# Optimization experiments

Hardware: AMD Instinct MI355X
Metric: run time of the kernel (lower is better)

Reference implementation:

```python
import jax, jax.numpy as jnp
import numpy as np

IN_FEATURES = 28 * 28  # 784
OUT_FEATURES = 1000    # label_num
GRID_SIZE = 10
SPLINE_ORDER = 3
GRID_RANGE = (0.0, 1.0)


def _make_grid(dtype):
    # grid = arange(-spline_order, grid_size+spline_order+1) * h + grid_range[0]
    h = (GRID_RANGE[1] - GRID_RANGE[0]) / GRID_SIZE
    return (jnp.arange(-SPLINE_ORDER, GRID_SIZE + SPLINE_ORDER + 1, dtype=dtype) * h
            + GRID_RANGE[0])  # [grid_size + 2*spline_order + 1] = [17]


def b_splines(x):
    # x: [B, in]; returns [B, in, grid_size + spline_order] = [B, 784, 13]
    grid = _make_grid(x.dtype)
    g = grid[None, None, :]          # broadcast over batch and in_features
    xu = x[:, :, None]               # [B, in, 1]
    bases = ((xu >= g[..., :-1]) & (xu < g[..., 1:])).astype(x.dtype)
    for k in range(1, SPLINE_ORDER + 1):
        left = (xu - g[..., :-(k + 1)]) / (g[..., k:-1] - g[..., :-(k + 1)])
        right = (g[..., k + 1:] - xu) / (g[..., k + 1:] - g[..., 1:-k])
        bases = left * bases[..., :-1] + right * bases[..., 1:]
    return bases


def setup_inputs() -> dict:
    key = jax.random.key(0)
    k1, k2, k3, k4 = jax.random.split(key, 4)
    B = 8192
    x = jax.random.uniform(k1, (B, 1, 28, 28), dtype=jnp.float32)  # values in grid range [0,1]
    base_weight = 0.03 * jax.random.normal(k2, (OUT_FEATURES, IN_FEATURES), dtype=jnp.float32)
    spline_weight = 0.02 * jax.random.normal(
        k3, (OUT_FEATURES, IN_FEATURES, GRID_SIZE + SPLINE_ORDER), dtype=jnp.float32)
    spline_scaler = 1.0 + 0.05 * jax.random.normal(k4, (OUT_FEATURES, IN_FEATURES), dtype=jnp.float32)
    return {"x": x, "base_weight": base_weight,
            "spline_weight": spline_weight, "spline_scaler": spline_scaler}


def reference(x, base_weight, spline_weight, spline_scaler):
    B = x.shape[0]
    xf = x.reshape(B, IN_FEATURES)                       # Flatten
    # base branch: SiLU(x) @ base_weight.T
    base_out = jnp.einsum('bi,oi->bo', jax.nn.silu(xf), base_weight)
    # spline branch: B-spline basis contracted with scaled spline weights
    bases = b_splines(xf)                                # [B, in, 13]
    sw = spline_weight * spline_scaler[..., None]        # [out, in, 13]
    spline_out = jnp.einsum('big,oig->bo', bases, sw)
    logits = base_out + spline_out                       # [B, out]
    return jax.nn.log_softmax(logits, axis=1)
```

## Files before the change

### kernel.cpp

```cpp
#include <hip/hip_runtime.h>
#include <hip/hip_bf16.h>
#include <stdint.h>

#define IN_F 784
#define OUT_F 1000
#define CH 16
#define KDIM (IN_F * CH)
#define MDIM 8192
#define NPAD 1024
#define KSTEPS (KDIM / 64)

typedef __attribute__((ext_vector_type(8))) short bf16x8;
typedef __attribute__((ext_vector_type(4))) float f32x4;

__device__ __forceinline__ unsigned short f2bf(float f) {
    unsigned u = __float_as_uint(f);
    u = (u + 0x7FFFu + ((u >> 16) & 1u)) >> 16;
    return (unsigned short)u;
}
__device__ __forceinline__ unsigned pack2(float lo, float hi) {
    return (unsigned)f2bf(lo) | ((unsigned)f2bf(hi) << 16);
}

__global__ void prep_A(const float* __restrict__ X, unsigned short* __restrict__ A) {
    int tid = blockIdx.x * 256 + threadIdx.x;
    int b = tid / IN_F;
    int i = tid - b * IN_F;
    float x = X[tid];
    float s = x / (1.0f + __expf(-x));
    float tf = x * 10.0f;
    float cf = floorf(tf);
    cf = fminf(fmaxf(cf, 0.0f), 9.0f);
    int c = (int)cf;
    float u = tf - cf;
    float u2 = u * u, u3 = u2 * u;
    float om = 1.0f - u;
    const float s6 = 1.0f / 6.0f;
    float b0 = om * om * om * s6;
    float b1 = (3.0f * u3 - 6.0f * u2 + 4.0f) * s6;
    float b2 = (-3.0f * u3 + 3.0f * u2 + 3.0f * u + 1.0f) * s6;
    float b3 = u3 * s6;
    float v[16];
    v[0] = s;
    #pragma unroll
    for (int k = 0; k < 13; ++k) {
        float val = (k == c)     ? b0 : 0.0f;
        val       = (k == c + 1) ? b1 : val;
        val       = (k == c + 2) ? b2 : val;
        val       = (k == c + 3) ? b3 : val;
        v[1 + k] = val;
    }
    v[14] = 0.0f; v[15] = 0.0f;
    unsigned w[8];
    #pragma unroll
    for (int j = 0; j < 8; ++j) w[j] = pack2(v[2 * j], v[2 * j + 1]);
    uint4* dst = (uint4*)(A + (size_t)b * KDIM + (size_t)i * CH);
    dst[0] = make_uint4(w[0], w[1], w[2], w[3]);
    dst[1] = make_uint4(w[4], w[5], w[6], w[7]);
}

__global__ void prep_W(const float* __restrict__ BW, const float* __restrict__ SW,
                       const float* __restrict__ SC, unsigned short* __restrict__ Wm) {
    int tid = blockIdx.x * 256 + threadIdx.x;
    int o = tid / IN_F;
    int i = tid - o * IN_F;
    unsigned w[8];
    if (o < OUT_F) {
        float bw = BW[o * IN_F + i];
        float sc = SC[o * IN_F + i];
        const float* swp = SW + (size_t)(o * IN_F + i) * 13;
        float v[16];
        v[0] = bw;
        #pragma unroll
        for (int g = 0; g < 13; ++g) v[1 + g] = swp[g] * sc;
        v[14] = 0.0f; v[15] = 0.0f;
        #pragma unroll
        for (int j = 0; j < 8; ++j) w[j] = pack2(v[2 * j], v[2 * j + 1]);
    } else {
        #pragma unroll
        for (int j = 0; j < 8; ++j) w[j] = 0u;
    }
    uint4* dst = (uint4*)(Wm + (size_t)o * KDIM + (size_t)i * CH);
    dst[0] = make_uint4(w[0], w[1], w[2], w[3]);
    dst[1] = make_uint4(w[4], w[5], w[6], w[7]);
}

__global__ void __launch_bounds__(256) kan_gemm(const unsigned short* __restrict__ A,
                                                const unsigned short* __restrict__ W,
                                                float* __restrict__ out) {
    __shared__ __align__(16) unsigned char smem[32768];
    const int t = threadIdx.x;
    const int bid = blockIdx.x;
    const int mb = bid >> 3, nb = bid & 7;
    const int bRow = mb * 128, bCol = nb * 128;
    const int w = t >> 6;
    const int lane = t & 63;
    const int lrow = lane & 15;
    const int lk = lane >> 4;
    const int sx = lrow & 7;
    const int r8 = t >> 3;
    const int p = t & 7;
    const int wm = w >> 1, wn = w & 1;

    const char* Ab = (const char*)A;
    const char* Wb = (const char*)W;

    f32x4 acc[4][4];
    #pragma unroll
    for (int m = 0; m < 4; ++m)
        #pragma unroll
        for (int n = 0; n < 4; ++n)
            acc[m][n] = (f32x4){0.f, 0.f, 0.f, 0.f};

    for (int ks = 0; ks < KSTEPS; ++ks) {
        const int k0 = ks * 64;
        #pragma unroll
        for (int it = 0; it < 4; ++it) {
            int r = it * 32 + r8;
            int sc = p ^ (r & 7);
            const char* src = Ab + ((size_t)(bRow + r) * KDIM + k0) * 2 + sc * 16;
            __builtin_amdgcn_global_load_lds(
                (const __attribute__((address_space(1))) char*)src,
                (__attribute__((address_space(3))) char*)&smem[it * 4096 + w * 1024],
                16, 0, 0);
        }
        #pragma unroll
        for (int it = 0; it < 4; ++it) {
            int r = it * 32 + r8;
            int sc = p ^ (r & 7);
            const char* src = Wb + ((size_t)(bCol + r) * KDIM + k0) * 2 + sc * 16;
            __builtin_amdgcn_global_load_lds(
                (const __attribute__((address_space(1))) char*)src,
                (__attribute__((address_space(3))) char*)&smem[16384 + it * 4096 + w * 1024],
                16, 0, 0);
        }
        __syncthreads();

        #pragma unroll
        for (int kk = 0; kk < 2; ++kk) {
            bf16x8 af[4], bfr[4];
            #pragma unroll
            for (int m = 0; m < 4; ++m) {
                int row = wm * 64 + m * 16 + lrow;
                int ch = (kk * 4 + lk) ^ sx;
                af[m] = *(const bf16x8*)&smem[row * 128 + ch * 16];
            }
            #pragma unroll
            for (int n = 0; n < 4; ++n) {
                int row = wn * 64 + n * 16 + lrow;
                int ch = (kk * 4 + lk) ^ sx;
                bfr[n] = *(const bf16x8*)&smem[16384 + row * 128 + ch * 16];
            }
            #pragma unroll
            for (int m = 0; m < 4; ++m)
                #pragma unroll
                for (int n = 0; n < 4; ++n)
                    acc[m][n] = __builtin_amdgcn_mfma_f32_16x16x32_bf16(af[m], bfr[n], acc[m][n], 0, 0, 0);
        }
        __syncthreads();
    }

    #pragma unroll
    for (int m = 0; m < 4; ++m) {
        int grow0 = bRow + wm * 64 + m * 16 + lk * 4;
        #pragma unroll
        for (int n = 0; n < 4; ++n) {
            int gcol = bCol + wn * 64 + n * 16 + lrow;
            if (gcol < OUT_F) {
                #pragma unroll
                for (int j = 0; j < 4; ++j)
                    out[(size_t)(grow0 + j) * OUT_F + gcol] = acc[m][n][j];
            }
        }
    }
}

__global__ void logsoftmax_inplace(float* __restrict__ out) {
    const int b = blockIdx.x;
    float* row = out + (size_t)b * OUT_F;
    const int t = threadIdx.x;
    const int ln = t & 63, wv = t >> 6;
    float v[4];
    #pragma unroll
    for (int j = 0; j < 4; ++j) {
        int idx = t + 256 * j;
        v[j] = (idx < OUT_F) ? row[idx] : -1e30f;
    }
    float m = fmaxf(fmaxf(v[0], v[1]), fmaxf(v[2], v[3]));
    #pragma unroll
    for (int off = 32; off > 0; off >>= 1) m = fmaxf(m, __shfl_xor(m, off, 64));
    __shared__ float red[4];
    if (ln == 0) red[wv] = m;
    __syncthreads();
    m = fmaxf(fmaxf(red[0], red[1]), fmaxf(red[2], red[3]));
    float s = 0.f;
    #pragma unroll
    for (int j = 0; j < 4; ++j) {
        int idx = t + 256 * j;
        if (idx < OUT_F) s += __expf(v[j] - m);
    }
    #pragma unroll
    for (int off = 32; off > 0; off >>= 1) s += __shfl_xor(s, off, 64);
    __syncthreads();
    if (ln == 0) red[wv] = s;
    __syncthreads();
    s = red[0] + red[1] + red[2] + red[3];
    float lse = m + logf(s);
    #pragma unroll
    for (int j = 0; j < 4; ++j) {
        int idx = t + 256 * j;
        if (idx < OUT_F) row[idx] = v[j] - lse;
    }
}

extern "C" void kernel_launch(void* const* d_in, const int* in_sizes, int n_in,
                              void* d_out, int out_size, void* d_ws, size_t ws_size,
                              hipStream_t stream) {
    const float* x  = (const float*)d_in[0];
    const float* bw = (const float*)d_in[1];
    const float* sw = (const float*)d_in[2];
    const float* sc = (const float*)d_in[3];
    float* out = (float*)d_out;

    unsigned short* A  = (unsigned short*)d_ws;
    unsigned short* Wm = (unsigned short*)((char*)d_ws + (size_t)MDIM * KDIM * 2);

    prep_A<<<dim3(MDIM * IN_F / 256), 256, 0, stream>>>(x, A);
    prep_W<<<dim3(NPAD * IN_F / 256), 256, 0, stream>>>(bw, sw, sc, Wm);
    kan_gemm<<<dim3((MDIM / 128) * (NPAD / 128)), 256, 0, stream>>>(A, Wm, out);
    logsoftmax_inplace<<<dim3(MDIM), 256, 0, stream>>>(out);
}
```

Measured before the change: 462.2 us.

## Split GEMM K-loop across two warp groups per block with LDS reduction

The GEMM block grows to 512 threads, with two 256-thread groups each handling half of the K range in its own 32KB LDS region. The partial accumulators are summed through LDS before the store. The block-to-tile mapping is also remapped so consecutive blocks share the same N column tile, which should improve L2 reuse of W. The goal is more warps per CU to hide load latency, at the cost of double LDS use, which may lower the number of resident blocks, plus a reduction epilogue.

```diff
diff --git a/kernel.cpp b/kernel.cpp
--- a/kernel.cpp
+++ b/kernel.cpp
@@ -9,6 +9,7 @@
 #define MDIM 8192
 #define NPAD 1024
 #define KSTEPS (KDIM / 64)
+#define KHALF (KSTEPS / 2)
 
 typedef __attribute__((ext_vector_type(8))) short bf16x8;
 typedef __attribute__((ext_vector_type(4))) float f32x4;
@@ -85,22 +86,27 @@
     dst[1] = make_uint4(w[4], w[5], w[6], w[7]);
 }
 
-__global__ void __launch_bounds__(256) kan_gemm(const unsigned short* __restrict__ A,
-                                                const unsigned short* __restrict__ W,
-                                                float* __restrict__ out) {
-    __shared__ __align__(16) unsigned char smem[32768];
+__global__ void __launch_bounds__(512, 4) kan_gemm(const unsigned short* __restrict__ A,
+                                                   const unsigned short* __restrict__ W,
+                                                   float* __restrict__ out) {
+    __shared__ __align__(16) unsigned char smem[65536];
     const int t = threadIdx.x;
     const int bid = blockIdx.x;
-    const int mb = bid >> 3, nb = bid & 7;
+    const int sid = (bid & 7) * 64 + (bid >> 3);
+    const int mb = sid >> 3, nb = sid & 7;
     const int bRow = mb * 128, bCol = nb * 128;
-    const int w = t >> 6;
+
+    const int g  = t >> 8;
+    const int tg = t & 255;
+    const int wg = tg >> 6;
     const int lane = t & 63;
     const int lrow = lane & 15;
     const int lk = lane >> 4;
     const int sx = lrow & 7;
-    const int r8 = t >> 3;
-    const int p = t & 7;
-    const int wm = w >> 1, wn = w & 1;
+    const int r8 = tg >> 3;
+    const int p = tg & 7;
+    const int wm = wg >> 1, wn = wg & 1;
+    const int sbase = g * 32768;
 
     const char* Ab = (const char*)A;
     const char* Wb = (const char*)W;
@@ -112,8 +118,8 @@
         for (int n = 0; n < 4; ++n)
             acc[m][n] = (f32x4){0.f, 0.f, 0.f, 0.f};
 
-    for (int ks = 0; ks < KSTEPS; ++ks) {
-        const int k0 = ks * 64;
+    for (int ks = 0; ks < KHALF; ++ks) {
+        const int k0 = (g * KHALF + ks) * 64;
         #pragma unroll
         for (int it = 0; it < 4; ++it) {
             int r = it * 32 + r8;
@@ -121,7 +127,7 @@
             const char* src = Ab + ((size_t)(bRow + r) * KDIM + k0) * 2 + sc * 16;
             __builtin_amdgcn_global_load_lds(
                 (const __attribute__((address_space(1))) char*)src,
-                (__attribute__((address_space(3))) char*)&smem[it * 4096 + w * 1024],
+                (__attribute__((address_space(3))) char*)&smem[sbase + it * 4096 + wg * 1024],
                 16, 0, 0);
         }
         #pragma unroll
@@ -131,7 +137,7 @@
             const char* src = Wb + ((size_t)(bCol + r) * KDIM + k0) * 2 + sc * 16;
             __builtin_amdgcn_global_load_lds(
                 (const __attribute__((address_space(1))) char*)src,
-                (__attribute__((address_space(3))) char*)&smem[16384 + it * 4096 + w * 1024],
+                (__attribute__((address_space(3))) char*)&smem[sbase + 16384 + it * 4096 + wg * 1024],
                 16, 0, 0);
         }
         __syncthreads();
@@ -143,13 +149,13 @@
             for (int m = 0; m < 4; ++m) {
                 int row = wm * 64 + m * 16 + lrow;
                 int ch = (kk * 4 + lk) ^ sx;
-                af[m] = *(const bf16x8*)&smem[row * 128 + ch * 16];
+                af[m] = *(const bf16x8*)&smem[sbase + row * 128 + ch * 16];
             }
             #pragma unroll
             for (int n = 0; n < 4; ++n) {
                 int row = wn * 64 + n * 16 + lrow;
                 int ch = (kk * 4 + lk) ^ sx;
-                bfr[n] = *(const bf16x8*)&smem[16384 + row * 128 + ch * 16];
+                bfr[n] = *(const bf16x8*)&smem[sbase + 16384 + row * 128 + ch * 16];
             }
             #pragma unroll
             for (int m = 0; m < 4; ++m)
@@ -160,16 +166,33 @@
         __syncthreads();
     }
 
-    #pragma unroll
-    for (int m = 0; m < 4; ++m) {
-        int grow0 = bRow + wm * 64 + m * 16 + lk * 4;
-        #pragma unroll
-        for (int n = 0; n < 4; ++n) {
-            int gcol = bCol + wn * 64 + n * 16 + lrow;
-            if (gcol < OUT_F) {
-                #pragma unroll
-                for (int j = 0; j < 4; ++j)
-                    out[(size_t)(grow0 + j) * OUT_F + gcol] = acc[m][n][j];
+    if (g == 1) {
+        #pragma unroll
+        for (int m = 0; m < 4; ++m)
+            #pragma unroll
+            for (int n = 0; n < 4; ++n)
+                *(f32x4*)&smem[wg * 16384 + (m * 4 + n) * 1024 + lane * 16] = acc[m][n];
+    }
+    __syncthreads();
+    if (g == 0) {
+        #pragma unroll
+        for (int m = 0; m < 4; ++m)
+            #pragma unroll
+            for (int n = 0; n < 4; ++n) {
+                f32x4 o = *(const f32x4*)&smem[wg * 16384 + (m * 4 + n) * 1024 + lane * 16];
+                acc[m][n] += o;
+            }
+        #pragma unroll
+        for (int m = 0; m < 4; ++m) {
+            int grow0 = bRow + wm * 64 + m * 16 + lk * 4;
+            #pragma unroll
+            for (int n = 0; n < 4; ++n) {
+                int gcol = bCol + wn * 64 + n * 16 + lrow;
+                if (gcol < OUT_F) {
+                    #pragma unroll
+                    for (int j = 0; j < 4; ++j)
+                        out[(size_t)(grow0 + j) * OUT_F + gcol] = acc[m][n][j];
+                }
             }
         }
     }
@@ -227,6 +250,6 @@
 
     prep_A<<<dim3(MDIM * IN_F / 256), 256, 0, stream>>>(x, A);
     prep_W<<<dim3(NPAD * IN_F / 256), 256, 0, stream>>>(bw, sw, sc, Wm);
-    kan_gemm<<<dim3((MDIM / 128) * (NPAD / 128)), 256, 0, stream>>>(A, Wm, out);
+    kan_gemm<<<dim3((MDIM / 128) * (NPAD / 128)), 512, 0, stream>>>(A, Wm, out);
     logsoftmax_inplace<<<dim3(MDIM), 256, 0, stream>>>(out);
 }
```

Result: faster. 442.0 us (-4.4%).

## Triple-buffer GEMM LDS loads with 256x128 tiles and grouped block order

Applied to the files above, without the earlier changes.

Restructures the GEMM to use 512-thread blocks computing 256x128 tiles, with a three-stage LDS ring buffer so global-to-LDS loads run two k-steps ahead of the MFMA work. One barrier per iteration replaces the two __syncthreads, gated by explicit vmcnt waits. Block IDs are remapped so blocks sharing a W column tile run together for cache reuse, and the MFMA section runs at raised wave priority. Using 144KB of LDS per block limits occupancy, and the hand-written vmcnt counting must match the number of outstanding loads exactly.

```diff
diff --git a/kernel.cpp b/kernel.cpp
--- a/kernel.cpp
+++ b/kernel.cpp
@@ -8,7 +8,8 @@
 #define KDIM (IN_F * CH)
 #define MDIM 8192
 #define NPAD 1024
-#define KSTEPS (KDIM / 64)
+#define NT (KDIM / 64)
+#define BUFSZ 49152
 
 typedef __attribute__((ext_vector_type(8))) short bf16x8;
 typedef __attribute__((ext_vector_type(4))) float f32x4;
@@ -85,25 +86,51 @@
     dst[1] = make_uint4(w[4], w[5], w[6], w[7]);
 }
 
-__global__ void __launch_bounds__(256) kan_gemm(const unsigned short* __restrict__ A,
-                                                const unsigned short* __restrict__ W,
-                                                float* __restrict__ out) {
-    __shared__ __align__(16) unsigned char smem[32768];
+__global__ void __launch_bounds__(512, 2) kan_gemm(const unsigned short* __restrict__ A,
+                                                   const unsigned short* __restrict__ W,
+                                                   float* __restrict__ out) {
+    __shared__ __align__(16) unsigned char smem[3 * BUFSZ];
     const int t = threadIdx.x;
     const int bid = blockIdx.x;
-    const int mb = bid >> 3, nb = bid & 7;
-    const int bRow = mb * 128, bCol = nb * 128;
-    const int w = t >> 6;
+    const int sid = ((bid & 7) << 5) + (bid >> 3);
+    const int mb = sid >> 3, nb = sid & 7;
+    const int bRow = mb << 8, bCol = nb << 7;
+
     const int lane = t & 63;
+    const int w    = t >> 6;
     const int lrow = lane & 15;
-    const int lk = lane >> 4;
-    const int sx = lrow & 7;
-    const int r8 = t >> 3;
-    const int p = t & 7;
-    const int wm = w >> 1, wn = w & 1;
-
-    const char* Ab = (const char*)A;
-    const char* Wb = (const char*)W;
+    const int lk   = lane >> 4;
+    const int sx   = lrow & 7;
+    const int wm   = w >> 1, wn = w & 1;
+    const int r8   = t >> 3;
+    const int p    = t & 7;
+    const int lch  = p ^ (r8 & 7);
+
+    const char* srcA[4];
+    const char* srcB[2];
+    #pragma unroll
+    for (int it = 0; it < 4; ++it)
+        srcA[it] = (const char*)A + ((size_t)(bRow + it * 64 + r8) * KDIM) * 2 + lch * 16;
+    #pragma unroll
+    for (int it = 0; it < 2; ++it)
+        srcB[it] = (const char*)W + ((size_t)(bCol + it * 64 + r8) * KDIM) * 2 + lch * 16;
+
+    auto stage = [&](int kt, int buf) {
+        const size_t ko = (size_t)kt << 7;
+        const unsigned db = buf * BUFSZ + t * 16;
+        #pragma unroll
+        for (int it = 0; it < 4; ++it)
+            __builtin_amdgcn_global_load_lds(
+                (const __attribute__((address_space(1))) char*)(srcA[it] + ko),
+                (__attribute__((address_space(3))) char*)&smem[db + it * 8192],
+                16, 0, 0);
+        #pragma unroll
+        for (int it = 0; it < 2; ++it)
+            __builtin_amdgcn_global_load_lds(
+                (const __attribute__((address_space(1))) char*)(srcB[it] + ko),
+                (__attribute__((address_space(3))) char*)&smem[db + 32768 + it * 8192],
+                16, 0, 0);
+    };
 
     f32x4 acc[4][4];
     #pragma unroll
@@ -112,60 +139,57 @@
         for (int n = 0; n < 4; ++n)
             acc[m][n] = (f32x4){0.f, 0.f, 0.f, 0.f};
 
-    for (int ks = 0; ks < KSTEPS; ++ks) {
-        const int k0 = ks * 64;
-        #pragma unroll
-        for (int it = 0; it < 4; ++it) {
-            int r = it * 32 + r8;
-            int sc = p ^ (r & 7);
-            const char* src = Ab + ((size_t)(bRow + r) * KDIM + k0) * 2 + sc * 16;
-            __builtin_amdgcn_global_load_lds(
-                (const __attribute__((address_space(1))) char*)src,
-                (__attribute__((address_space(3))) char*)&smem[it * 4096 + w * 1024],
-                16, 0, 0);
+    stage(0, 0);
+    stage(1, 1);
+
+    int cur = 0;
+    int nbf = 2;
+    for (int kt = 0; kt < NT; ++kt) {
+        if (kt < NT - 1) asm volatile("s_waitcnt vmcnt(6)" ::: "memory");
+        else             asm volatile("s_waitcnt vmcnt(0)" ::: "memory");
+        __builtin_amdgcn_s_barrier();
+        asm volatile("" ::: "memory");
+
+        const unsigned char* Abuf = &smem[cur * BUFSZ];
+        const unsigned char* Bbuf = Abuf + 32768;
+        bf16x8 af[4][2], bfr[4][2];
+        #pragma unroll
+        for (int m = 0; m < 4; ++m) {
+            const int row = (wm << 6) + (m << 4) + lrow;
+            #pragma unroll
+            for (int kk = 0; kk < 2; ++kk)
+                af[m][kk] = *(const bf16x8*)&Abuf[row * 128 + (((kk << 2) + lk) ^ sx) * 16];
         }
         #pragma unroll
-        for (int it = 0; it < 4; ++it) {
-            int r = it * 32 + r8;
-            int sc = p ^ (r & 7);
-            const char* src = Wb + ((size_t)(bCol + r) * KDIM + k0) * 2 + sc * 16;
-            __builtin_amdgcn_global_load_lds(
-                (const __attribute__((address_space(1))) char*)src,
-                (__attribute__((address_space(3))) char*)&smem[16384 + it * 4096 + w * 1024],
-                16, 0, 0);
+        for (int n = 0; n < 4; ++n) {
+            const int row = (wn << 6) + (n << 4) + lrow;
+            #pragma unroll
+            for (int kk = 0; kk < 2; ++kk)
+                bfr[n][kk] = *(const bf16x8*)&Bbuf[row * 128 + (((kk << 2) + lk) ^ sx) * 16];
         }
-        __syncthreads();
-
-        #pragma unroll
-        for (int kk = 0; kk < 2; ++kk) {
-            bf16x8 af[4], bfr[4];
-            #pragma unroll
-            for (int m = 0; m < 4; ++m) {
-                int row = wm * 64 + m * 16 + lrow;
-                int ch = (kk * 4 + lk) ^ sx;
-                af[m] = *(const bf16x8*)&smem[row * 128 + ch * 16];
-            }
+
+        if (kt + 2 < NT) stage(kt + 2, nbf);
+
+        __builtin_amdgcn_s_setprio(1);
+        #pragma unroll
+        for (int m = 0; m < 4; ++m)
             #pragma unroll
             for (int n = 0; n < 4; ++n) {
-                int row = wn * 64 + n * 16 + lrow;
-                int ch = (kk * 4 + lk) ^ sx;
-                bfr[n] = *(const bf16x8*)&smem[16384 + row * 128 + ch * 16];
+                acc[m][n] = __builtin_amdgcn_mfma_f32_16x16x32_bf16(af[m][0], bfr[n][0], acc[m][n], 0, 0, 0);
+                acc[m][n] = __builtin_amdgcn_mfma_f32_16x16x32_bf16(af[m][1], bfr[n][1], acc[m][n], 0, 0, 0);
             }
-            #pragma unroll
-            for (int m = 0; m < 4; ++m)
-                #pragma unroll
-                for (int n = 0; n < 4; ++n)
-                    acc[m][n] = __builtin_amdgcn_mfma_f32_16x16x32_bf16(af[m], bfr[n], acc[m][n], 0, 0, 0);
-        }
-        __syncthreads();
+        __builtin_amdgcn_s_setprio(0);
+
+        cur = (cur == 2) ? 0 : cur + 1;
+        nbf = (nbf == 2) ? 0 : nbf + 1;
     }
 
     #pragma unroll
     for (int m = 0; m < 4; ++m) {
-        int grow0 = bRow + wm * 64 + m * 16 + lk * 4;
+        int grow0 = bRow + (wm << 6) + (m << 4) + (lk << 2);
         #pragma unroll
         for (int n = 0; n < 4; ++n) {
-            int gcol = bCol + wn * 64 + n * 16 + lrow;
+            int gcol = bCol + (wn << 6) + (n << 4) + lrow;
             if (gcol < OUT_F) {
                 #pragma unroll
                 for (int j = 0; j < 4; ++j)
@@ -227,6 +251,6 @@
 
     prep_A<<<dim3(MDIM * IN_F / 256), 256, 0, stream>>>(x, A);
     prep_W<<<dim3(NPAD * IN_F / 256), 256, 0, stream>>>(bw, sw, sc, Wm);
-    kan_gemm<<<dim3((MDIM / 128) * (NPAD / 128)), 256, 0, stream>>>(A, Wm, out);
+    kan_gemm<<<dim3((MDIM / 256) * (NPAD / 128)), 512, 0, stream>>>(A, Wm, out);
     logsoftmax_inplace<<<dim3(MDIM), 256, 0, stream>>>(out);
 }
```

Measured after the change: 373.4 us. 19.2% less time.
